# Kernel tuning notes

Hardware: AMD Instinct MI355X
Metric: run time of the kernel (lower is better)

Reference implementation:

```python
import jax, jax.numpy as jnp
import numpy as np


def setup_inputs() -> dict:
    key = jax.random.key(0)
    k1, k2, k3, k4 = jax.random.split(key, 4)
    dim, hidden_dim = 256, 16
    B, Q = 8, 300
    pos = jax.random.uniform(k1, (B, Q, 4), dtype=jnp.float32)  # xywh in [0,1)
    queries = jax.random.normal(k2, (B, Q, dim), dtype=jnp.float32)
    # weight_generator: Linear(dim, 4*hidden_dim+1)
    Wg = jax.random.normal(k3, (dim, 4 * hidden_dim + 1), dtype=jnp.float32) * (1.0 / np.sqrt(dim))
    bg = jax.random.normal(k4, (4 * hidden_dim + 1,), dtype=jnp.float32) * 0.01
    return {"pos": pos, "queries": queries, "Wg": Wg, "bg": bg, "size": 64}


def _box_brpb(weights, pos, hidden_dim, H, W):
    # weights: [N, 4h+1], pos: [N, 4] (cx, cy, w, h)
    h = hidden_dim
    N = weights.shape[0]
    w1 = weights[:, : 2 * h].reshape(N, 2, h)      # first-layer weights for (x, y)
    b1 = weights[:, 2 * h : 3 * h]                 # [N, h]
    w2 = weights[:, 3 * h : 4 * h]                 # [N, h]
    b2 = weights[:, 4 * h]                         # [N]

    cx, cy, bw, bh = pos[:, 0], pos[:, 1], pos[:, 2], pos[:, 3]
    xs = (jnp.arange(W, dtype=weights.dtype) + 0.5) / W   # [W]
    ys = (jnp.arange(H, dtype=weights.dtype) + 0.5) / H   # [H]
    # relative coords normalized by box size: [N, W] and [N, H]
    rel_x = (xs[None, :] - cx[:, None]) / bw[:, None]
    rel_y = (ys[None, :] - cy[:, None]) / bh[:, None]

    # hidden pre-activation: [N, H, W, h]
    pre = (rel_x[:, None, :, None] * w1[:, 0][:, None, None, :]
           + rel_y[:, :, None, None] * w1[:, 1][:, None, None, :]
           + b1[:, None, None, :])
    act = jax.nn.relu(pre)
    out = jnp.einsum('nhwk,nk->nhw', act, w2) + b2[:, None, None]
    return out  # [N, H, W]


def reference(pos, queries, Wg, bg, size):
    hidden_dim = 16
    H = W = int(size)
    batch_shape = pos.shape[:-1]
    pos_f = pos.reshape(-1, 4)
    q_f = queries.reshape(-1, queries.shape[-1])
    weights = q_f @ Wg + bg                     # [N, 4h+1]
    out = _box_brpb(weights, pos_f, hidden_dim, H, W)
    return out.reshape(batch_shape + (H, W))
```

## Files before the change

### kernel.cpp

```cpp
#include <hip/hip_runtime.h>

#define HD  16
#define DIM 256
#define NW  65
#define HW  64

__global__ __launch_bounds__(256, 4) void posmlp_kernel(
    const float* __restrict__ pos,
    const float* __restrict__ queries,
    const float* __restrict__ Wg,
    const float* __restrict__ bg,
    float* __restrict__ out)
{
    const int n   = blockIdx.x;
    const int tid = threadIdx.x;

    __shared__ float qs[DIM];
    __shared__ float wl[NW];

    qs[tid] = queries[n * DIM + tid];
    __syncthreads();

    if (tid < NW) {
        float a0 = 0.f, a1 = 0.f, a2 = 0.f, a3 = 0.f;
        #pragma unroll 4
        for (int d = 0; d < DIM; d += 4) {
            a0 = fmaf(qs[d + 0], Wg[(d + 0) * NW + tid], a0);
            a1 = fmaf(qs[d + 1], Wg[(d + 1) * NW + tid], a1);
            a2 = fmaf(qs[d + 2], Wg[(d + 2) * NW + tid], a2);
            a3 = fmaf(qs[d + 3], Wg[(d + 3) * NW + tid], a3);
        }
        wl[tid] = bg[tid] + ((a0 + a1) + (a2 + a3));
    }
    __syncthreads();

    const float cx = pos[n * 4 + 0];
    const float cy = pos[n * 4 + 1];
    const float inv_bw = 1.0f / pos[n * 4 + 2];
    const float inv_bh = 1.0f / pos[n * 4 + 3];

    float w1x[HD], w1y[HD], b1[HD], w2[HD];
    #pragma unroll
    for (int k = 0; k < HD; ++k) {
        w1x[k] = wl[k];
        w1y[k] = wl[HD + k];
        b1[k]  = wl[2 * HD + k];
        w2[k]  = wl[3 * HD + k];
    }
    const float b2 = wl[4 * HD];

    const int xg = tid & 15;
    const int yl = tid >> 4;
    const int x0 = xg * 4;

    float rx[4];
    #pragma unroll
    for (int j = 0; j < 4; ++j)
        rx[j] = ((x0 + j + 0.5f) * (1.0f / HW) - cx) * inv_bw;

    float* outn = out + (size_t)n * (HW * HW);

    #pragma unroll
    for (int it = 0; it < 4; ++it) {
        const int y = it * 16 + yl;
        const float ry = ((y + 0.5f) * (1.0f / HW) - cy) * inv_bh;

        float ayb[HD];
        #pragma unroll
        for (int k = 0; k < HD; ++k)
            ayb[k] = fmaf(ry, w1y[k], b1[k]);

        float4 acc = make_float4(b2, b2, b2, b2);
        #pragma unroll
        for (int k = 0; k < HD; ++k) {
            const float t0 = fmaxf(fmaf(rx[0], w1x[k], ayb[k]), 0.0f);
            const float t1 = fmaxf(fmaf(rx[1], w1x[k], ayb[k]), 0.0f);
            const float t2 = fmaxf(fmaf(rx[2], w1x[k], ayb[k]), 0.0f);
            const float t3 = fmaxf(fmaf(rx[3], w1x[k], ayb[k]), 0.0f);
            acc.x = fmaf(t0, w2[k], acc.x);
            acc.y = fmaf(t1, w2[k], acc.y);
            acc.z = fmaf(t2, w2[k], acc.z);
            acc.w = fmaf(t3, w2[k], acc.w);
        }
        *reinterpret_cast<float4*>(outn + y * HW + x0) = acc;
    }
}

extern "C" void kernel_launch(void* const* d_in, const int* in_sizes, int n_in,
                              void* d_out, int out_size, void* d_ws, size_t ws_size,
                              hipStream_t stream) {
    const float* pos = (const float*)d_in[0];
    const float* q   = (const float*)d_in[1];
    const float* Wg  = (const float*)d_in[2];
    const float* bg  = (const float*)d_in[3];
    float* out = (float*)d_out;

    const int N = in_sizes[0] / 4;
    posmlp_kernel<<<N, 256, 0, stream>>>(pos, q, Wg, bg, out);
}
```

Baseline: 96.23 us.

## Split weight-generation GEMV into separate fully-parallel kernel, render with scalar loads

Moves the per-query linear projection out of the render kernel into its own kernel where every thread computes one output weight, instead of only 65 of 256 threads working while the rest wait at a barrier. The render kernel then reads the 65 weights from workspace using readfirstlane so they live in scalar registers, with no shared memory or syncthreads. Occupancy hint is raised to 8 blocks. The cost is an extra kernel launch and a global round-trip for the weight workspace.

Result: slower. 102.6 us (+6.6%).

```diff
diff --git a/kernel.cpp b/kernel.cpp
--- a/kernel.cpp
+++ b/kernel.cpp
@@ -5,49 +5,62 @@
 #define NW  65
 #define HW  64
 
-__global__ __launch_bounds__(256, 4) void posmlp_kernel(
-    const float* __restrict__ pos,
+__global__ __launch_bounds__(256, 8) void weights_kernel(
     const float* __restrict__ queries,
     const float* __restrict__ Wg,
     const float* __restrict__ bg,
+    float* __restrict__ W,
+    int total)
+{
+    const int idx = blockIdx.x * 256 + threadIdx.x;
+    if (idx >= total) return;
+    const unsigned n = (unsigned)idx / NW;
+    const int j = idx - (int)n * NW;
+
+    const float4* q4  = reinterpret_cast<const float4*>(queries + (size_t)n * DIM);
+    const float*  wgj = Wg + j;
+
+    float a0 = 0.f, a1 = 0.f, a2 = 0.f, a3 = 0.f;
+    #pragma unroll 4
+    for (int d4 = 0; d4 < DIM / 4; ++d4) {
+        const float4 qv = q4[d4];
+        const int d = d4 * 4;
+        a0 = fmaf(qv.x, wgj[(d + 0) * NW], a0);
+        a1 = fmaf(qv.y, wgj[(d + 1) * NW], a1);
+        a2 = fmaf(qv.z, wgj[(d + 2) * NW], a2);
+        a3 = fmaf(qv.w, wgj[(d + 3) * NW], a3);
+    }
+    W[idx] = bg[j] + ((a0 + a1) + (a2 + a3));
+}
+
+__device__ __forceinline__ float uload(const float* p) {
+    return __int_as_float(__builtin_amdgcn_readfirstlane(__float_as_int(*p)));
+}
+
+__global__ __launch_bounds__(256, 8) void render_kernel(
+    const float* __restrict__ pos,
+    const float* __restrict__ W,
     float* __restrict__ out)
 {
     const int n   = blockIdx.x;
     const int tid = threadIdx.x;
 
-    __shared__ float qs[DIM];
-    __shared__ float wl[NW];
+    const float* wn = W + (size_t)n * NW;
 
-    qs[tid] = queries[n * DIM + tid];
-    __syncthreads();
-
-    if (tid < NW) {
-        float a0 = 0.f, a1 = 0.f, a2 = 0.f, a3 = 0.f;
-        #pragma unroll 4
-        for (int d = 0; d < DIM; d += 4) {
-            a0 = fmaf(qs[d + 0], Wg[(d + 0) * NW + tid], a0);
-            a1 = fmaf(qs[d + 1], Wg[(d + 1) * NW + tid], a1);
-            a2 = fmaf(qs[d + 2], Wg[(d + 2) * NW + tid], a2);
-            a3 = fmaf(qs[d + 3], Wg[(d + 3) * NW + tid], a3);
-        }
-        wl[tid] = bg[tid] + ((a0 + a1) + (a2 + a3));
-    }
-    __syncthreads();
-
-    const float cx = pos[n * 4 + 0];
-    const float cy = pos[n * 4 + 1];
-    const float inv_bw = 1.0f / pos[n * 4 + 2];
-    const float inv_bh = 1.0f / pos[n * 4 + 3];
+    const float cx     = uload(pos + n * 4 + 0);
+    const float cy     = uload(pos + n * 4 + 1);
+    const float inv_bw = 1.0f / uload(pos + n * 4 + 2);
+    const float inv_bh = 1.0f / uload(pos + n * 4 + 3);
 
     float w1x[HD], w1y[HD], b1[HD], w2[HD];
     #pragma unroll
     for (int k = 0; k < HD; ++k) {
-        w1x[k] = wl[k];
-        w1y[k] = wl[HD + k];
-        b1[k]  = wl[2 * HD + k];
-        w2[k]  = wl[3 * HD + k];
+        w1x[k] = uload(wn + k);
+        w1y[k] = uload(wn + HD + k);
+        b1[k]  = uload(wn + 2 * HD + k);
+        w2[k]  = uload(wn + 3 * HD + k);
     }
-    const float b2 = wl[4 * HD];
+    const float b2 = uload(wn + 4 * HD);
 
     const int xg = tid & 15;
     const int yl = tid >> 4;
@@ -96,5 +109,9 @@
     float* out = (float*)d_out;
 
     const int N = in_sizes[0] / 4;
-    posmlp_kernel<<<N, 256, 0, stream>>>(pos, q, Wg, bg, out);
+    const int total = N * NW;
+    float* W = (float*)d_ws;
+
+    weights_kernel<<<(total + 255) / 256, 256, 0, stream>>>(q, Wg, bg, W, total);
+    render_kernel<<<N, 256, 0, stream>>>(pos, W, out);
 }
```
